# Kernel tuning notes

Measured on AMD Instinct MI355X. Metric: run time of the kernel, lower is better.

Reference implementation:

```python
import jax, jax.numpy as jnp
import numpy as np

B, S, DIM, H, C = 1, 1024, 4096, 32, 8
HD = DIM // H  # 128
NEG = -1e9


def setup_inputs() -> dict:
    key = jax.random.key(0)
    ks = jax.random.split(key, 8)
    scale = 0.02
    x = jax.random.normal(ks[0], (B, S, DIM), jnp.float32)
    wq = jax.random.normal(ks[1], (DIM, DIM), jnp.float32) * scale
    wk = jax.random.normal(ks[2], (DIM, DIM), jnp.float32) * scale
    wv = jax.random.normal(ks[3], (DIM, DIM), jnp.float32) * scale
    wo = jax.random.normal(ks[4], (DIM, DIM), jnp.float32) * scale
    # RoPE tables (theta=10000), matching precompute_freqs_cis
    inv = 1.0 / (10000.0 ** (np.arange(0, HD, 2, dtype=np.float32) / HD))  # [HD/2]
    ang = np.arange(S, dtype=np.float32)[:, None] * inv[None, :]  # [S, HD/2]
    freqs_cos = jnp.asarray(np.cos(ang))
    freqs_sin = jnp.asarray(np.sin(ang))
    # causal mask used at prefill (start_pos == 0)
    mask = jnp.where(jnp.triu(jnp.ones((S, S), bool), k=1), jnp.float32(NEG), 0.0)
    # cluster labels: ensure every cluster non-empty; rep = first head with label
    rng = np.random.default_rng(0)
    lab = np.concatenate([np.arange(C), rng.integers(0, C, H - C)]).astype(np.int32)
    rep = np.array([np.where(lab == c)[0][0] for c in range(C)], dtype=np.int32)
    return {
        "x": x, "wq": wq, "wk": wk, "wv": wv, "wo": wo,
        "freqs_cos": freqs_cos, "freqs_sin": freqs_sin, "mask": mask,
        "cluster_assignment": jnp.asarray(lab), "rep_heads": jnp.asarray(rep),
        "start_pos": 0,
    }


def _rope(x, cos, sin):
    # x: [b, s, h, d]; cos/sin: [s, d/2]; interleaved complex multiply
    xr, xi = x[..., ::2], x[..., 1::2]
    cos = cos[None, :, None, :]
    sin = sin[None, :, None, :]
    orr = xr * cos - xi * sin
    oi = xr * sin + xi * cos
    return jnp.stack([orr, oi], axis=-1).reshape(x.shape)


def reference(x, wq, wk, wv, wo, freqs_cos, freqs_sin, mask,
              cluster_assignment, rep_heads, start_pos):
    b, s, dim = x.shape
    h, d = H, HD
    xq = (x @ wq.T).reshape(b, s, h, d)
    xk = (x @ wk.T).reshape(b, s, h, d)
    xv = (x @ wv.T).reshape(b, s, h, d)
    xq = _rope(xq, freqs_cos, freqs_sin)
    xk = _rope(xk, freqs_cos, freqs_sin)
    xqh = jnp.transpose(xq, (0, 2, 1, 3))  # [b, h, s, d]
    xkh = jnp.transpose(xk, (0, 2, 1, 3))
    vh = jnp.transpose(xv, (0, 2, 1, 3))
    # CHAI: gather representative head per cluster, score once per cluster
    xq_new = xqh[:, rep_heads]  # [b, C, s, d]
    xk_new = xkh[:, rep_heads]
    sc = jnp.einsum("bcqd,bckd->bcqk", xq_new, xk_new) / jnp.sqrt(jnp.float32(d))
    # scatter cluster scores back to every member head (pure gather by label)
    scores = sc[:, cluster_assignment]  # [b, h, s, s]
    scores = scores + mask[None, None]
    p = jax.nn.softmax(scores.astype(jnp.float32), axis=-1).astype(x.dtype)
    out = jnp.einsum("bhqk,bhkd->bhqd", p, vh)
    out = jnp.transpose(out, (0, 2, 1, 3)).reshape(b, s, h * d)
    return out @ wo.T
```

## Files before the change

kernel.cpp:

```cpp
#include <hip/hip_runtime.h>

typedef __bf16 bf16x8 __attribute__((ext_vector_type(8)));
typedef float f32x4 __attribute__((ext_vector_type(4)));
typedef unsigned short u16x8 __attribute__((ext_vector_type(8)));

#define BM 128
#define BN 128
#define BK 64

__device__ __forceinline__ unsigned short f2bf(float f) {
    union { float f; unsigned int u; } x; x.f = f;
    unsigned int u = x.u;
    u += 0x7fffu + ((u >> 16) & 1u);
    return (unsigned short)(u >> 16);
}

__device__ __forceinline__ float bf2f(unsigned short h) {
    union { unsigned int u; float f; } x; x.u = ((unsigned int)h) << 16;
    return x.f;
}

__device__ __forceinline__ void async_copy16(const void* g, void* l) {
    __builtin_amdgcn_global_load_lds(
        (const __attribute__((address_space(1))) void*)(uintptr_t)g,
        (__attribute__((address_space(3))) void*)(uintptr_t)l, 16, 0, 0);
}

__global__ void cvt_all(const float* __restrict__ x, const float* __restrict__ wq,
                        const float* __restrict__ wk, const float* __restrict__ wv,
                        const float* __restrict__ wo, const int* __restrict__ rep,
                        unsigned short* __restrict__ xb, unsigned short* __restrict__ wqkvb,
                        unsigned short* __restrict__ wob) {
    const long total = 5767168;
    long stride = (long)gridDim.x * 256;
    for (long i = (long)blockIdx.x * 256 + threadIdx.x; i < total; i += stride) {
        const float* src;
        unsigned short* dst;
        if (i < 524288) {
            src = x + i * 8;
            dst = xb + i * 8;
        } else if (i < 3670016) {
            long j = i - 524288;
            int r = (int)(j >> 9), c8 = (int)(j & 511);
            const float* s;
            if (r < 1024)      s = wq + ((long)(rep[r >> 7] * 128 + (r & 127)) << 12);
            else if (r < 2048) s = wk + ((long)(rep[(r - 1024) >> 7] * 128 + (r & 127)) << 12);
            else               s = wv + ((long)(r - 2048) << 12);
            src = s + c8 * 8;
            dst = wqkvb + ((long)r << 12) + c8 * 8;
        } else {
            long j = i - 3670016;
            src = wo + j * 8;
            dst = wob + j * 8;
        }
        const f32x4* p4 = (const f32x4*)src;
        f32x4 v0 = __builtin_nontemporal_load(p4);
        f32x4 v1 = __builtin_nontemporal_load(p4 + 1);
        u16x8 o = { f2bf(v0[0]), f2bf(v0[1]), f2bf(v0[2]), f2bf(v0[3]),
                    f2bf(v1[0]), f2bf(v1[1]), f2bf(v1[2]), f2bf(v1[3]) };
        *(u16x8*)dst = o;
    }
}

template<int MODE>
__global__ __launch_bounds__(256, 2) void gemm_bt(
    const unsigned short* __restrict__ A, const unsigned short* __restrict__ B,
    unsigned short* __restrict__ C, int K, int lda, int ldb, int ldc,
    long long aZ, long long bZ, long long cZ, const int* __restrict__ aIdx,
    int kOffZ, int nby) {
    __shared__ unsigned short As[2][BM * BK];
    __shared__ unsigned short Bs[2][BN * BK];

    int L = blockIdx.x;
    int q8 = gridDim.x >> 3;
    int wk_ = (L & 7) * q8 + (L >> 3);
    int bmi = wk_ & 7;
    int t2 = wk_ >> 3;
    int bni = t2 % nby;
    int z = t2 / nby;

    if (MODE == 1 && bni > bmi) return;

    A += (aIdx ? (long long)aIdx[z] : (long long)z) * aZ;
    B += (long long)z * bZ;
    int bm = bmi * BM;
    int bn = bni * BN;
    int t = threadIdx.x;
    int lane = t & 63;
    int w = t >> 6;
    int wr = (w >> 1) * 64, wc = (w & 1) * 64;

    int kt0 = (MODE == 0) ? z * kOffZ : 0;
    int kEnd = kt0 + ((MODE == 2) ? min(K, bm + BM) : K);

#define STAGE(buf, kt) \
    _Pragma("unroll") \
    for (int i = 0; i < 4; ++i) { \
        int f = i * 256 + t; \
        int row = f >> 3, c8 = f & 7; \
        int cs = c8 ^ (row & 7); \
        async_copy16(A + (long)(bm + row) * lda + (kt) + cs * 8, &As[buf][f * 8]); \
        async_copy16(B + (long)(bn + row) * ldb + (kt) + cs * 8, &Bs[buf][f * 8]); \
    }

    f32x4 acc[4][4] = {};

    STAGE(0, kt0);
    asm volatile("s_waitcnt vmcnt(0)" ::: "memory");
    __syncthreads();

    int cur = 0;
    for (int kt = kt0; kt < kEnd; kt += BK) {
        if (kt + BK < kEnd) { STAGE(cur ^ 1, kt + BK); }

        const unsigned short* Asc = As[cur];
        const unsigned short* Bsc = Bs[cur];
#pragma unroll
        for (int kk = 0; kk < BK; kk += 32) {
            bf16x8 a[4], b[4];
            int r0 = lane & 15;
            int kof = kk + ((lane >> 4) << 3);
            int kc = kof >> 3;
#pragma unroll
            for (int m = 0; m < 4; ++m) {
                int ra = wr + m * 16 + r0;
                a[m] = *(const bf16x8*)&Asc[ra * 64 + ((kc ^ (ra & 7)) << 3)];
            }
#pragma unroll
            for (int n = 0; n < 4; ++n) {
                int rb = wc + n * 16 + r0;
                b[n] = *(const bf16x8*)&Bsc[rb * 64 + ((kc ^ (rb & 7)) << 3)];
            }
#pragma unroll
            for (int m = 0; m < 4; ++m)
#pragma unroll
                for (int n = 0; n < 4; ++n)
                    acc[m][n] = __builtin_amdgcn_mfma_f32_16x16x32_bf16(a[m], b[n], acc[m][n], 0, 0, 0);
        }
        asm volatile("s_waitcnt vmcnt(0)" ::: "memory");
        __syncthreads();
        cur ^= 1;
    }
#undef STAGE

    int cl = lane & 15;
    int rbase = (lane >> 4) << 2;
    unsigned short* Cp = C + (long long)z * cZ;
#pragma unroll
    for (int m = 0; m < 4; ++m)
#pragma unroll
        for (int n = 0; n < 4; ++n)
#pragma unroll
            for (int j = 0; j < 4; ++j)
                Cp[(long)(bm + wr + m * 16 + rbase + j) * ldc + (bn + wc + n * 16 + cl)] = f2bf(acc[m][n][j]);
}

__global__ void reduce_rope(unsigned short* __restrict__ qkv,
                            const float* __restrict__ fc, const float* __restrict__ fs,
                            int nsplit) {
    int s = blockIdx.y;
    int cc = (blockIdx.x * 256 + threadIdx.x) * 8;
    long base = (long)s * 6144 + cc;
    ushort4 a0 = *(const ushort4*)(qkv + base);
    ushort4 a1 = *(const ushort4*)(qkv + base + 4);
    float f[8] = { bf2f(a0.x), bf2f(a0.y), bf2f(a0.z), bf2f(a0.w),
                   bf2f(a1.x), bf2f(a1.y), bf2f(a1.z), bf2f(a1.w) };
    for (int z = 1; z < nsplit; ++z) {
        const unsigned short* p = qkv + (long)z * 6291456;
        ushort4 b0 = *(const ushort4*)(p + base);
        ushort4 b1 = *(const ushort4*)(p + base + 4);
        f[0] += bf2f(b0.x); f[1] += bf2f(b0.y); f[2] += bf2f(b0.z); f[3] += bf2f(b0.w);
        f[4] += bf2f(b1.x); f[5] += bf2f(b1.y); f[6] += bf2f(b1.z); f[7] += bf2f(b1.w);
    }
    if (cc < 2048) {
        int i0 = (cc & 127) >> 1;
        const float* cp = fc + (s << 6) + i0;
        const float* sp = fs + (s << 6) + i0;
#pragma unroll
        for (int p = 0; p < 4; ++p) {
            float co = cp[p], sn = sp[p];
            float x0 = f[2 * p], x1 = f[2 * p + 1];
            f[2 * p] = x0 * co - x1 * sn;
            f[2 * p + 1] = x0 * sn + x1 * co;
        }
    }
    ushort4 o0 = { f2bf(f[0]), f2bf(f[1]), f2bf(f[2]), f2bf(f[3]) };
    ushort4 o1 = { f2bf(f[4]), f2bf(f[5]), f2bf(f[6]), f2bf(f[7]) };
    *(ushort4*)(qkv + base) = o0;
    *(ushort4*)(qkv + base + 4) = o1;
}

__global__ void reduce_out4(const unsigned short* __restrict__ p, float* __restrict__ out) {
    long i = (long)blockIdx.x * 256 + threadIdx.x;
    ushort4 a = ((const ushort4*)p)[i];
    ushort4 b = ((const ushort4*)(p + 4194304))[i];
    ushort4 c = ((const ushort4*)(p + 8388608))[i];
    ushort4 d = ((const ushort4*)(p + 12582912))[i];
    float4 o;
    o.x = bf2f(a.x) + bf2f(b.x) + bf2f(c.x) + bf2f(d.x);
    o.y = bf2f(a.y) + bf2f(b.y) + bf2f(c.y) + bf2f(d.y);
    o.z = bf2f(a.z) + bf2f(b.z) + bf2f(c.z) + bf2f(d.z);
    o.w = bf2f(a.w) + bf2f(b.w) + bf2f(c.w) + bf2f(d.w);
    ((float4*)out)[i] = o;
}

__global__ void transpose_v(const unsigned short* __restrict__ qkv, unsigned short* __restrict__ vt) {
    __shared__ unsigned short tile[32][33];
    int h = blockIdx.z, d0 = blockIdx.x * 32, s0 = blockIdx.y * 32;
    int tx = threadIdx.x & 31, ty = threadIdx.x >> 5;
#pragma unroll
    for (int i = 0; i < 32; i += 8)
        tile[ty + i][tx] = qkv[(long)(s0 + ty + i) * 6144 + 2048 + h * 128 + d0 + tx];
    __syncthreads();
#pragma unroll
    for (int i = 0; i < 32; i += 8)
        vt[(long)h * 131072 + (long)(d0 + ty + i) * 1024 + s0 + tx] = tile[tx][ty + i];
}

__global__ __launch_bounds__(256) void softmax_causal(const unsigned short* __restrict__ sc,
                                                      unsigned short* __restrict__ P) {
    int i = blockIdx.x;
    int c = blockIdx.y;
    long base = ((long)c << 20) + ((long)i << 10);
    const unsigned short* row = sc + base;
    unsigned short* prow = P + base;
    int t = threadIdx.x;
    const float alpha = 0.08838834764831845f;
    int nj = i >> 8;

    float v[4];
    float mx = -3.4e38f;
    for (int j0 = 0; j0 <= nj; ++j0) {
        int j = j0 * 256 + t;
        float x = bf2f(row[j]) * alpha;
        v[j0] = (j <= i) ? x : -3.4e38f;
        mx = fmaxf(mx, v[j0]);
    }
#pragma unroll
    for (int o = 32; o > 0; o >>= 1) mx = fmaxf(mx, __shfl_xor(mx, o));
    __shared__ float red[4];
    int w = t >> 6, lane = t & 63;
    if (lane == 0) red[w] = mx;
    __syncthreads();
    mx = fmaxf(fmaxf(red[0], red[1]), fmaxf(red[2], red[3]));

    float e[4];
    float sum = 0.f;
    for (int j0 = 0; j0 <= nj; ++j0) {
        e[j0] = (v[j0] > -1e37f) ? __expf(v[j0] - mx) : 0.f;
        sum += e[j0];
    }
#pragma unroll
    for (int o = 32; o > 0; o >>= 1) sum += __shfl_xor(sum, o);
    __syncthreads();
    if (lane == 0) red[w] = sum;
    __syncthreads();
    sum = red[0] + red[1] + red[2] + red[3];
    float inv = 1.f / sum;
    for (int j0 = 0; j0 <= nj; ++j0) {
        int j = j0 * 256 + t;
        prow[j] = f2bf(e[j0] * inv);
    }
}


extern "C" void kernel_launch(void* const* d_in, const int* in_sizes, int n_in,
                              void* d_out, int out_size, void* d_ws, size_t ws_size,
                              hipStream_t stream) {
    const float* x  = (const float*)d_in[0];
    const float* wq = (const float*)d_in[1];
    const float* wk = (const float*)d_in[2];
    const float* wv = (const float*)d_in[3];
    const float* wo = (const float*)d_in[4];
    const float* fc = (const float*)d_in[5];
    const float* fs = (const float*)d_in[6];
    const int* lab = (const int*)d_in[8];
    const int* rep = (const int*)d_in[9];
    float* out = (float*)d_out;

    char* ws = (char*)d_ws;
    unsigned short* xb    = (unsigned short*)(ws);
    unsigned short* wqkvb = (unsigned short*)(ws + 8388608);
    unsigned short* wob   = (unsigned short*)(ws + 58720256);
    unsigned short* qkv_s = (unsigned short*)(ws + 92274688);
    unsigned short* vt    = (unsigned short*)(ws + 104857600);
    unsigned short* scores= (unsigned short*)(ws + 8388608);
    unsigned short* P     = (unsigned short*)(ws + 41943040);
    unsigned short* opart = (unsigned short*)(ws + 8388608);
    unsigned short* attn  = xb;

    int skQ = (ws_size >= (size_t)117440512) ? 2 : 1;

    cvt_all<<<2048, 256, 0, stream>>>(x, wq, wk, wv, wo, rep, xb, wqkvb, wob);

    if (skQ == 2) {
        gemm_bt<0><<<768, 256, 0, stream>>>(
            xb, wqkvb, qkv_s, 2048, 4096, 4096, 6144, 0, 0, 6291456, nullptr, 2048, 48);
    } else {
        gemm_bt<0><<<384, 256, 0, stream>>>(
            xb, wqkvb, qkv_s, 4096, 4096, 4096, 6144, 0, 0, 0, nullptr, 0, 48);
    }

    reduce_rope<<<dim3(3, 1024), 256, 0, stream>>>(qkv_s, fc, fs, skQ);
    transpose_v<<<dim3(4, 32, 32), 256, 0, stream>>>(qkv_s, vt);

    gemm_bt<1><<<512, 256, 0, stream>>>(
        qkv_s, qkv_s + 1024, scores, 128, 6144, 6144, 1024,
        128, 128, 1048576, nullptr, 0, 8);

    softmax_causal<<<dim3(1024, 8), 256, 0, stream>>>(scores, P);

    gemm_bt<2><<<256, 256, 0, stream>>>(
        P, vt, attn, 1024, 1024, 1024, 4096,
        1048576, 131072, 128, lab, 0, 1);

    gemm_bt<0><<<1024, 256, 0, stream>>>(
        attn, wob, opart, 1024, 4096, 4096, 4096, 0, 0, 4194304, nullptr, 1024, 32);
    reduce_out4<<<4096, 256, 0, stream>>>(opart, out);
}
```

Before: 209.4 us.

## Overlap wo conversion with PV GEMM and tighten GEMM pipeline barriers

The fp32-to-bf16 conversion of wo moves out of the upfront cvt kernel into extra blocks of the PV GEMM launch, so it runs alongside the attention matmul. The GEMM main loop now waits only for the previous stage's loads (vmcnt(8)) and uses raw s_barrier with sched_barrier, which lets the next tile's prefetch overlap compute. The output projection drops from a 4-way to a 2-way split-K, halving the partial-sum reduction. The QKV split-K reduction for V moves into transpose_v, so reduce_rope only touches the Q/K columns, and vt is relocated in the workspace. These cut launch and memory traffic but rely on exact waitcnt counts and workspace aliasing being correct.

```diff
diff --git a/kernel.cpp b/kernel.cpp
--- a/kernel.cpp
+++ b/kernel.cpp
@@ -28,10 +28,9 @@
 
 __global__ void cvt_all(const float* __restrict__ x, const float* __restrict__ wq,
                         const float* __restrict__ wk, const float* __restrict__ wv,
-                        const float* __restrict__ wo, const int* __restrict__ rep,
-                        unsigned short* __restrict__ xb, unsigned short* __restrict__ wqkvb,
-                        unsigned short* __restrict__ wob) {
-    const long total = 5767168;
+                        const int* __restrict__ rep,
+                        unsigned short* __restrict__ xb, unsigned short* __restrict__ wqkvb) {
+    const long total = 3670016;
     long stride = (long)gridDim.x * 256;
     for (long i = (long)blockIdx.x * 256 + threadIdx.x; i < total; i += stride) {
         const float* src;
@@ -39,7 +38,7 @@
         if (i < 524288) {
             src = x + i * 8;
             dst = xb + i * 8;
-        } else if (i < 3670016) {
+        } else {
             long j = i - 524288;
             int r = (int)(j >> 9), c8 = (int)(j & 511);
             const float* s;
@@ -48,10 +47,6 @@
             else               s = wv + ((long)(r - 2048) << 12);
             src = s + c8 * 8;
             dst = wqkvb + ((long)r << 12) + c8 * 8;
-        } else {
-            long j = i - 3670016;
-            src = wo + j * 8;
-            dst = wob + j * 8;
         }
         const f32x4* p4 = (const f32x4*)src;
         f32x4 v0 = __builtin_nontemporal_load(p4);
@@ -67,12 +62,26 @@
     const unsigned short* __restrict__ A, const unsigned short* __restrict__ B,
     unsigned short* __restrict__ C, int K, int lda, int ldb, int ldc,
     long long aZ, long long bZ, long long cZ, const int* __restrict__ aIdx,
-    int kOffZ, int nby) {
+    int kOffZ, int nby, const float* __restrict__ woF, unsigned short* __restrict__ wobD) {
     __shared__ unsigned short As[2][BM * BK];
     __shared__ unsigned short Bs[2][BN * BK];
 
     int L = blockIdx.x;
-    int q8 = gridDim.x >> 3;
+    if (MODE == 3 && L >= 256) {
+        long i0 = (long)(L - 256) * 256 + threadIdx.x;
+        for (long i = i0; i < 2097152; i += 131072) {
+            const f32x4* p4 = (const f32x4*)(woF + i * 8);
+            f32x4 v0 = __builtin_nontemporal_load(p4);
+            f32x4 v1 = __builtin_nontemporal_load(p4 + 1);
+            u16x8 o = { f2bf(v0[0]), f2bf(v0[1]), f2bf(v0[2]), f2bf(v0[3]),
+                        f2bf(v1[0]), f2bf(v1[1]), f2bf(v1[2]), f2bf(v1[3]) };
+            *(u16x8*)(wobD + i * 8) = o;
+        }
+        return;
+    }
+
+    int nblk = (MODE == 3) ? 256 : gridDim.x;
+    int q8 = nblk >> 3;
     int wk_ = (L & 7) * q8 + (L >> 3);
     int bmi = wk_ & 7;
     int t2 = wk_ >> 3;
@@ -91,7 +100,8 @@
     int wr = (w >> 1) * 64, wc = (w & 1) * 64;
 
     int kt0 = (MODE == 0) ? z * kOffZ : 0;
-    int kEnd = kt0 + ((MODE == 2) ? min(K, bm + BM) : K);
+    int kLen = (MODE >= 2) ? min(K, bm + BM) : K;
+    int nIter = kLen / BK;
 
 #define STAGE(buf, kt) \
     _Pragma("unroll") \
@@ -106,12 +116,15 @@
     f32x4 acc[4][4] = {};
 
     STAGE(0, kt0);
-    asm volatile("s_waitcnt vmcnt(0)" ::: "memory");
-    __syncthreads();
-
     int cur = 0;
-    for (int kt = kt0; kt < kEnd; kt += BK) {
-        if (kt + BK < kEnd) { STAGE(cur ^ 1, kt + BK); }
+    for (int it = 0; it < nIter; ++it) {
+        if (it + 1 < nIter) {
+            STAGE(cur ^ 1, kt0 + (it + 1) * BK);
+            asm volatile("s_waitcnt vmcnt(8)\n\ts_barrier" ::: "memory");
+        } else {
+            asm volatile("s_waitcnt vmcnt(0)\n\ts_barrier" ::: "memory");
+        }
+        __builtin_amdgcn_sched_barrier(0);
 
         const unsigned short* Asc = As[cur];
         const unsigned short* Bsc = Bs[cur];
@@ -137,8 +150,8 @@
                 for (int n = 0; n < 4; ++n)
                     acc[m][n] = __builtin_amdgcn_mfma_f32_16x16x32_bf16(a[m], b[n], acc[m][n], 0, 0, 0);
         }
-        asm volatile("s_waitcnt vmcnt(0)" ::: "memory");
-        __syncthreads();
+        asm volatile("s_waitcnt lgkmcnt(0)\n\ts_barrier" ::: "memory");
+        __builtin_amdgcn_sched_barrier(0);
         cur ^= 1;
     }
 #undef STAGE
@@ -158,31 +171,29 @@
 __global__ void reduce_rope(unsigned short* __restrict__ qkv,
                             const float* __restrict__ fc, const float* __restrict__ fs,
                             int nsplit) {
-    int s = blockIdx.y;
-    int cc = (blockIdx.x * 256 + threadIdx.x) * 8;
+    int s = blockIdx.x;
+    int cc = threadIdx.x * 8;
     long base = (long)s * 6144 + cc;
     ushort4 a0 = *(const ushort4*)(qkv + base);
     ushort4 a1 = *(const ushort4*)(qkv + base + 4);
     float f[8] = { bf2f(a0.x), bf2f(a0.y), bf2f(a0.z), bf2f(a0.w),
                    bf2f(a1.x), bf2f(a1.y), bf2f(a1.z), bf2f(a1.w) };
-    for (int z = 1; z < nsplit; ++z) {
-        const unsigned short* p = qkv + (long)z * 6291456;
+    if (nsplit == 2) {
+        const unsigned short* p = qkv + 6291456;
         ushort4 b0 = *(const ushort4*)(p + base);
         ushort4 b1 = *(const ushort4*)(p + base + 4);
         f[0] += bf2f(b0.x); f[1] += bf2f(b0.y); f[2] += bf2f(b0.z); f[3] += bf2f(b0.w);
         f[4] += bf2f(b1.x); f[5] += bf2f(b1.y); f[6] += bf2f(b1.z); f[7] += bf2f(b1.w);
     }
-    if (cc < 2048) {
-        int i0 = (cc & 127) >> 1;
-        const float* cp = fc + (s << 6) + i0;
-        const float* sp = fs + (s << 6) + i0;
-#pragma unroll
-        for (int p = 0; p < 4; ++p) {
-            float co = cp[p], sn = sp[p];
-            float x0 = f[2 * p], x1 = f[2 * p + 1];
-            f[2 * p] = x0 * co - x1 * sn;
-            f[2 * p + 1] = x0 * sn + x1 * co;
-        }
+    int i0 = (cc & 127) >> 1;
+    const float* cp = fc + (s << 6) + i0;
+    const float* sp = fs + (s << 6) + i0;
+#pragma unroll
+    for (int p = 0; p < 4; ++p) {
+        float co = cp[p], sn = sp[p];
+        float x0 = f[2 * p], x1 = f[2 * p + 1];
+        f[2 * p] = x0 * co - x1 * sn;
+        f[2 * p + 1] = x0 * sn + x1 * co;
     }
     ushort4 o0 = { f2bf(f[0]), f2bf(f[1]), f2bf(f[2]), f2bf(f[3]) };
     ushort4 o1 = { f2bf(f[4]), f2bf(f[5]), f2bf(f[6]), f2bf(f[7]) };
@@ -190,27 +201,30 @@
     *(ushort4*)(qkv + base + 4) = o1;
 }
 
-__global__ void reduce_out4(const unsigned short* __restrict__ p, float* __restrict__ out) {
+__global__ void reduce_out2(const unsigned short* __restrict__ p, float* __restrict__ out) {
     long i = (long)blockIdx.x * 256 + threadIdx.x;
     ushort4 a = ((const ushort4*)p)[i];
     ushort4 b = ((const ushort4*)(p + 4194304))[i];
-    ushort4 c = ((const ushort4*)(p + 8388608))[i];
-    ushort4 d = ((const ushort4*)(p + 12582912))[i];
     float4 o;
-    o.x = bf2f(a.x) + bf2f(b.x) + bf2f(c.x) + bf2f(d.x);
-    o.y = bf2f(a.y) + bf2f(b.y) + bf2f(c.y) + bf2f(d.y);
-    o.z = bf2f(a.z) + bf2f(b.z) + bf2f(c.z) + bf2f(d.z);
-    o.w = bf2f(a.w) + bf2f(b.w) + bf2f(c.w) + bf2f(d.w);
+    o.x = bf2f(a.x) + bf2f(b.x);
+    o.y = bf2f(a.y) + bf2f(b.y);
+    o.z = bf2f(a.z) + bf2f(b.z);
+    o.w = bf2f(a.w) + bf2f(b.w);
     ((float4*)out)[i] = o;
 }
 
-__global__ void transpose_v(const unsigned short* __restrict__ qkv, unsigned short* __restrict__ vt) {
+__global__ void transpose_v(const unsigned short* __restrict__ qkv,
+                            unsigned short* __restrict__ vt, int nsplit) {
     __shared__ unsigned short tile[32][33];
     int h = blockIdx.z, d0 = blockIdx.x * 32, s0 = blockIdx.y * 32;
     int tx = threadIdx.x & 31, ty = threadIdx.x >> 5;
 #pragma unroll
-    for (int i = 0; i < 32; i += 8)
-        tile[ty + i][tx] = qkv[(long)(s0 + ty + i) * 6144 + 2048 + h * 128 + d0 + tx];
+    for (int i = 0; i < 32; i += 8) {
+        long idx = (long)(s0 + ty + i) * 6144 + 2048 + h * 128 + d0 + tx;
+        float v = bf2f(qkv[idx]);
+        if (nsplit == 2) v += bf2f(qkv[idx + 6291456]);
+        tile[ty + i][tx] = f2bf(v);
+    }
     __syncthreads();
 #pragma unroll
     for (int i = 0; i < 32; i += 8)
@@ -283,7 +297,7 @@
     unsigned short* wqkvb = (unsigned short*)(ws + 8388608);
     unsigned short* wob   = (unsigned short*)(ws + 58720256);
     unsigned short* qkv_s = (unsigned short*)(ws + 92274688);
-    unsigned short* vt    = (unsigned short*)(ws + 104857600);
+    unsigned short* vt    = (unsigned short*)(ws + 25165824);
     unsigned short* scores= (unsigned short*)(ws + 8388608);
     unsigned short* P     = (unsigned short*)(ws + 41943040);
     unsigned short* opart = (unsigned short*)(ws + 8388608);
@@ -291,30 +305,33 @@
 
     int skQ = (ws_size >= (size_t)117440512) ? 2 : 1;
 
-    cvt_all<<<2048, 256, 0, stream>>>(x, wq, wk, wv, wo, rep, xb, wqkvb, wob);
+    cvt_all<<<2048, 256, 0, stream>>>(x, wq, wk, wv, rep, xb, wqkvb);
 
     if (skQ == 2) {
         gemm_bt<0><<<768, 256, 0, stream>>>(
-            xb, wqkvb, qkv_s, 2048, 4096, 4096, 6144, 0, 0, 6291456, nullptr, 2048, 48);
+            xb, wqkvb, qkv_s, 2048, 4096, 4096, 6144, 0, 0, 6291456, nullptr, 2048, 48,
+            nullptr, nullptr);
     } else {
         gemm_bt<0><<<384, 256, 0, stream>>>(
-            xb, wqkvb, qkv_s, 4096, 4096, 4096, 6144, 0, 0, 0, nullptr, 0, 48);
-    }
-
-    reduce_rope<<<dim3(3, 1024), 256, 0, stream>>>(qkv_s, fc, fs, skQ);
-    transpose_v<<<dim3(4, 32, 32), 256, 0, stream>>>(qkv_s, vt);
+            xb, wqkvb, qkv_s, 4096, 4096, 4096, 6144, 0, 0, 0, nullptr, 0, 48,
+            nullptr, nullptr);
+    }
+
+    reduce_rope<<<1024, 256, 0, stream>>>(qkv_s, fc, fs, skQ);
+    transpose_v<<<dim3(4, 32, 32), 256, 0, stream>>>(qkv_s, vt, skQ);
 
     gemm_bt<1><<<512, 256, 0, stream>>>(
         qkv_s, qkv_s + 1024, scores, 128, 6144, 6144, 1024,
-        128, 128, 1048576, nullptr, 0, 8);
+        128, 128, 1048576, nullptr, 0, 8, nullptr, nullptr);
 
     softmax_causal<<<dim3(1024, 8), 256, 0, stream>>>(scores, P);
 
-    gemm_bt<2><<<256, 256, 0, stream>>>(
+    gemm_bt<3><<<768, 256, 0, stream>>>(
         P, vt, attn, 1024, 1024, 1024, 4096,
-        1048576, 131072, 128, lab, 0, 1);
-
-    gemm_bt<0><<<1024, 256, 0, stream>>>(
-        attn, wob, opart, 1024, 4096, 4096, 4096, 0, 0, 4194304, nullptr, 1024, 32);
-    reduce_out4<<<4096, 256, 0, stream>>>(opart, out);
-}
+        1048576, 131072, 128, lab, 0, 1, wo, wob);
+
+    gemm_bt<0><<<512, 256, 0, stream>>>(
+        attn, wob, opart, 2048, 4096, 4096, 4096, 0, 0, 4194304, nullptr, 2048, 32,
+        nullptr, nullptr);
+    reduce_out2<<<4096, 256, 0, stream>>>(opart, out);
+}
```

Result: faster. 199.6 us (-4.7%).
